# Performance work log

Measured on AMD Instinct MI355X. Metric: run time of the kernel, lower is better.

The kernel has to match this reference:

```python
import jax, jax.numpy as jnp
import numpy as np

B, N, F_IN, HID, OUT = 4096, 116, 116, 256, 2


def setup_inputs() -> dict:
    key = jax.random.key(0)
    ks = jax.random.split(key, 10)
    x = jax.random.normal(ks[0], (B, N, F_IN), dtype=jnp.float32)
    support = jax.random.uniform(ks[1], (B, N, N), dtype=jnp.float32) / N  # row-normalized-ish adjacency
    s = 0.05
    W1 = jax.random.normal(ks[2], (F_IN, HID), dtype=jnp.float32) * s
    b1 = jnp.zeros((HID,), dtype=jnp.float32)
    W2 = jax.random.normal(ks[3], (HID, OUT * 2), dtype=jnp.float32) * s
    b2 = jnp.zeros((OUT * 2,), dtype=jnp.float32)
    Wr1 = jax.random.normal(ks[4], (N * OUT * 2, 64), dtype=jnp.float32) * s
    br1 = jnp.zeros((64,), dtype=jnp.float32)
    Wr2 = jax.random.normal(ks[5], (64, OUT), dtype=jnp.float32) * s
    br2 = jnp.zeros((OUT,), dtype=jnp.float32)
    return {"x": x, "support": support, "W1": W1, "b1": b1, "W2": W2,
            "b2": b2, "Wr1": Wr1, "br1": br1, "Wr2": Wr2, "br2": br2}


def graph_conv(x, support, W, b):
    # GraphConv: activation(support @ (x @ W) + b)
    xw = jnp.einsum('bnf,fh->bnh', x, W)
    h = jnp.einsum('bnm,bmh->bnh', support, xw) + b
    return jax.nn.relu(h)


def reference(x, support, W1, b1, W2, b2, Wr1, br1, Wr2, br2):
    h = graph_conv(x, support, W1, b1)          # [B, N, HID]
    h = graph_conv(h, support, W2, b2)          # [B, N, 2*OUT]
    flat = h.reshape(h.shape[0], -1)            # [B, N*2*OUT]
    r = jax.nn.relu(flat @ Wr1 + br1)           # [B, 64]
    logits = r @ Wr2 + br2                      # [B, OUT]
    return jax.nn.log_softmax(logits, axis=-1)
```

## Files before the change

### kernel.cpp

```cpp
#include <hip/hip_runtime.h>
#include <math.h>


#define BDIM 512

constexpr int Bsz = 4096;
constexpr int Nn  = 116;
constexpr int Fin = 116;
constexpr int HID = 256;
constexpr int SK  = 136;
constexpr int NF4 = 3364;
constexpr int W1T_ELEMS = 256 * SK;
constexpr int W2T_OFF   = W1T_ELEMS;

typedef __bf16 bf16;
typedef __bf16 bf16x4 __attribute__((ext_vector_type(4)));
typedef __bf16 bf16x8 __attribute__((ext_vector_type(8)));
typedef float  floatx4 __attribute__((ext_vector_type(4)));


__global__ __launch_bounds__(1024) void prep_weights(
    const float* __restrict__ W1, const float* __restrict__ W2,
    bf16* __restrict__ WT)
{
  int j = blockIdx.x * 1024 + threadIdx.x;
  if (j < W1T_ELEMS) {
    int h = j / SK, kk = j - h * SK;
    WT[j] = (bf16)((kk < Fin) ? W1[kk * HID + h] : 0.f);
  } else if (j < W1T_ELEMS + 4 * 264) {
    int t = j - W1T_ELEMS;
    int n = t / 264, k = t - n * 264;
    WT[j] = (bf16)((k < HID) ? W2[k * 4 + n] : 0.f);
  }
}

__device__ __forceinline__ void gl2lds16(const void* g, void* l) {
  __builtin_amdgcn_global_load_lds(
      (const __attribute__((address_space(1))) void*)g,
      (__attribute__((address_space(3))) void*)l, 16, 0, 0);
}

__device__ __attribute__((always_inline)) inline void gemm128(
    const bf16* A, const bf16* Bt, floatx4 (&acc)[2][4],
    int wm, int wn, int quad, int l16)
{
#pragma unroll
  for (int ks = 0; ks < 4; ++ks) {
    const int k0 = ks * 32 + quad * 8;
    bf16x8 af[2], bfr[4];
#pragma unroll
    for (int mt = 0; mt < 2; ++mt)
      af[mt] = *(const bf16x8*)&A[(wm + mt * 16 + l16) * SK + k0];
#pragma unroll
    for (int nt = 0; nt < 4; ++nt)
      bfr[nt] = *(const bf16x8*)&Bt[(wn + nt * 16 + l16) * SK + k0];
#pragma unroll
    for (int mt = 0; mt < 2; ++mt)
#pragma unroll
      for (int nt = 0; nt < 4; ++nt)
        acc[mt][nt] = __builtin_amdgcn_mfma_f32_16x16x32_bf16(af[mt], bfr[nt], acc[mt][nt], 0, 0, 0);
  }
}

__device__ __attribute__((always_inline)) inline void gemm128_ra(
    const bf16x8 (&xf)[2][4], const bf16* Bt, floatx4 (&acc)[2][4],
    int wn, int quad, int l16)
{
#pragma unroll
  for (int ks = 0; ks < 4; ++ks) {
    const int k0 = ks * 32 + quad * 8;
    bf16x8 bfr[4];
#pragma unroll
    for (int nt = 0; nt < 4; ++nt)
      bfr[nt] = *(const bf16x8*)&Bt[(wn + nt * 16 + l16) * SK + k0];
#pragma unroll
    for (int mt = 0; mt < 2; ++mt)
#pragma unroll
      for (int nt = 0; nt < 4; ++nt)
        acc[mt][nt] = __builtin_amdgcn_mfma_f32_16x16x32_bf16(xf[mt][ks], bfr[nt], acc[mt][nt], 0, 0, 0);
  }
}

__device__ __attribute__((always_inline)) inline void zero_acc(floatx4 (&acc)[2][4])
{
#pragma unroll
  for (int mt = 0; mt < 2; ++mt)
#pragma unroll
    for (int nt = 0; nt < 4; ++nt) { acc[mt][nt][0]=acc[mt][nt][1]=acc[mt][nt][2]=acc[mt][nt][3]=0.f; }
}

__global__ __launch_bounds__(BDIM, 4) void gcn_fused(
    const float* __restrict__ X, const float* __restrict__ SUPP,
    const bf16* __restrict__ WT,
    const float* __restrict__ B1v, const float* __restrict__ B2v,
    const float* __restrict__ Wr1, const float* __restrict__ br1,
    const float* __restrict__ Wr2, const float* __restrict__ br2,
    float* __restrict__ OUTP)
{
  __shared__ __align__(16) bf16 ssup[128 * SK];
  __shared__ __align__(16) bf16 swb [128 * SK];
  __shared__ __align__(16) bf16 sw2t[4 * 264];
  __shared__ __align__(16) bf16 stt [4 * SK];
  __shared__ float sh2[464];
  __shared__ float spart[8 * 64];

  const int b    = blockIdx.x;
  const int tid  = threadIdx.x;
  const int wid  = tid >> 6;
  const int lane = tid & 63;
  const int quad = lane >> 4;
  const int l16  = lane & 15;

  const int wm = (wid & 3) * 32;
  const int wn = (wid >> 2) * 64;

  {
    const char* wg = (const char*)WT;
    char* wl = (char*)swb;
    for (int off = wid * 1024; off < 34816; off += 8 * 1024)
      gl2lds16(wg + off + lane * 16, wl + off);
    if (wid == 7) {
      const char* w2g = (const char*)(WT + W2T_OFF);
      char* w2l = (char*)sw2t;
      gl2lds16(w2g + lane * 16, w2l);
      gl2lds16(w2g + 1024 + lane * 16, w2l + 1024);
      if (lane < 4) gl2lds16(w2g + 2048 + lane * 16, w2l + 2048);
    }
  }

  const float* xrow = X + (size_t)b * (Nn * Fin);
  bf16x8 xf[2][4];
#pragma unroll
  for (int mt = 0; mt < 2; ++mt) {
    const int row = wm + mt * 16 + l16;
    const bool rv = row < Nn;
    const float* pr = xrow + (rv ? row : 0) * Fin;
#pragma unroll
    for (int ks = 0; ks < 4; ++ks) {
      const int k0 = ks * 32 + quad * 8;
      float4 u0 = make_float4(0.f, 0.f, 0.f, 0.f);
      float4 u1 = make_float4(0.f, 0.f, 0.f, 0.f);
      if (ks < 3 || quad < 3) u0 = *(const float4*)(pr + k0);
      if (ks < 3 || quad < 2) u1 = *(const float4*)(pr + k0 + 4);
      bf16x8 f;
      f[0]=(bf16)u0.x; f[1]=(bf16)u0.y; f[2]=(bf16)u0.z; f[3]=(bf16)u0.w;
      f[4]=(bf16)u1.x; f[5]=(bf16)u1.y; f[6]=(bf16)u1.z; f[7]=(bf16)u1.w;
      bf16x8 z; 
#pragma unroll
      for (int j = 0; j < 8; ++j) z[j] = (bf16)0.f;
      xf[mt][ks] = rv ? f : z;
    }
  }

  {
    const float4* sg = (const float4*)(SUPP + (size_t)b * (Nn * Nn));
    for (int i = tid; i < NF4; i += BDIM) {
      int m  = i / 29;
      int kq = (i - m * 29) * 4;
      float4 u = sg[i];
      bf16x4 q; q[0]=(bf16)u.x; q[1]=(bf16)u.y; q[2]=(bf16)u.z; q[3]=(bf16)u.w;
      *(bf16x4*)&ssup[m * SK + kq] = q;
    }
    bf16x4 z; z[0]=z[1]=z[2]=z[3]=(bf16)0.f;
    for (int i = tid; i < 128 * 5; i += BDIM) {
      int m = i / 5, cc = 116 + (i - m * 5) * 4;
      *(bf16x4*)&ssup[m * SK + cc] = z;
    }
    for (int i = tid; i < 12 * 29; i += BDIM) {
      int r = 116 + i / 29, cc = (i - (i / 29) * 29) * 4;
      *(bf16x4*)&ssup[r * SK + cc] = z;
    }
  }
  asm volatile("s_waitcnt vmcnt(0)" ::: "memory");
  __syncthreads();

  floatx4 acc[2][4];
  bf16x4  xwb0[2][4], xwb1[2][4];

  zero_acc(acc);
  gemm128_ra(xf, swb, acc, wn, quad, l16);
#pragma unroll
  for (int mt = 0; mt < 2; ++mt)
#pragma unroll
    for (int nt = 0; nt < 4; ++nt) {
      floatx4 a = acc[mt][nt];
      bf16x4 p; p[0]=(bf16)a[0]; p[1]=(bf16)a[1]; p[2]=(bf16)a[2]; p[3]=(bf16)a[3];
      xwb0[mt][nt] = p;
    }
  __syncthreads();

  {
    const char* wg = (const char*)(WT + 128 * SK);
    char* wl = (char*)swb;
    for (int off = wid * 1024; off < 34816; off += 8 * 1024)
      gl2lds16(wg + off + lane * 16, wl + off);
  }
  asm volatile("s_waitcnt vmcnt(0)" ::: "memory");
  __syncthreads();

  zero_acc(acc);
  gemm128_ra(xf, swb, acc, wn, quad, l16);
#pragma unroll
  for (int mt = 0; mt < 2; ++mt)
#pragma unroll
    for (int nt = 0; nt < 4; ++nt) {
      floatx4 a = acc[mt][nt];
      bf16x4 p; p[0]=(bf16)a[0]; p[1]=(bf16)a[1]; p[2]=(bf16)a[2]; p[3]=(bf16)a[3];
      xwb1[mt][nt] = p;
    }
  __syncthreads();

#pragma unroll
  for (int mt = 0; mt < 2; ++mt)
#pragma unroll
    for (int nt = 0; nt < 4; ++nt) {
      int mb = wm + mt * 16 + quad * 4;
      int n  = wn + nt * 16 + l16;
      *(bf16x4*)&swb[n * SK + mb] = xwb0[mt][nt];
    }
  __syncthreads();

  floatx4 acc3; acc3[0]=acc3[1]=acc3[2]=acc3[3]=0.f;

#pragma unroll
  for (int c = 0; c < 2; ++c) {
    zero_acc(acc);
    gemm128(ssup, swb, acc, wm, wn, quad, l16);
    __syncthreads();

#pragma unroll
    for (int mt = 0; mt < 2; ++mt)
#pragma unroll
      for (int nt = 0; nt < 4; ++nt) {
        int mb   = wm + mt * 16 + quad * 4;
        int coll = wn + nt * 16 + l16;
        float bb = B1v[c * 128 + coll];
        floatx4 a = acc[mt][nt];
#pragma unroll
        for (int r = 0; r < 4; ++r)
          swb[(mb + r) * SK + coll] = (bf16)fmaxf(a[r] + bb, 0.f);
      }
    __syncthreads();

#pragma unroll
    for (int ks = 0; ks < 4; ++ks) {
      const int k0 = ks * 32 + quad * 8;
      bf16x8 bfr = *(const bf16x8*)&sw2t[(l16 & 3) * 264 + c * 128 + k0];
      bf16x8 af  = *(const bf16x8*)&swb[(wid * 16 + l16) * SK + k0];
      acc3 = __builtin_amdgcn_mfma_f32_16x16x32_bf16(af, bfr, acc3, 0, 0, 0);
    }
    if (c == 0) {
      __syncthreads();
#pragma unroll
      for (int mt = 0; mt < 2; ++mt)
#pragma unroll
        for (int nt = 0; nt < 4; ++nt) {
          int mb = wm + mt * 16 + quad * 4;
          int n  = wn + nt * 16 + l16;
          *(bf16x4*)&swb[n * SK + mb] = xwb1[mt][nt];
        }
      __syncthreads();
    }
  }

  {
    int mb = wid * 16 + quad * 4;
    bf16x4 p;
    if (mb < Nn) { p[0]=(bf16)acc3[0]; p[1]=(bf16)acc3[1]; p[2]=(bf16)acc3[2]; p[3]=(bf16)acc3[3]; }
    else         { p[0]=p[1]=p[2]=p[3]=(bf16)0.f; }
    if (l16 < 4) *(bf16x4*)&stt[l16 * SK + mb] = p;
  }
  __syncthreads();

  floatx4 acc4; acc4[0]=acc4[1]=acc4[2]=acc4[3]=0.f;
#pragma unroll
  for (int ks = 0; ks < 4; ++ks) {
    const int k0 = ks * 32 + quad * 8;
    bf16x8 af  = *(const bf16x8*)&ssup[(wid * 16 + l16) * SK + k0];
    bf16x8 bfr = *(const bf16x8*)&stt[(l16 & 3) * SK + k0];
    acc4 = __builtin_amdgcn_mfma_f32_16x16x32_bf16(af, bfr, acc4, 0, 0, 0);
  }
  if (l16 < 4) {
    float bb = B2v[l16];
#pragma unroll
    for (int r = 0; r < 4; ++r) {
      int m = wid * 16 + quad * 4 + r;
      if (m < Nn) sh2[m * 4 + l16] = fmaxf(acc4[r] + bb, 0.f);
    }
  }
  __syncthreads();

  {
    int j   = tid & 63;
    int ksl = tid >> 6;
    int kb  = ksl * 58;
    float p = 0.f;
#pragma unroll 4
    for (int kk = 0; kk < 58; ++kk)
      p = fmaf(sh2[kb + kk], Wr1[(kb + kk) * 64 + j], p);
    spart[ksl * 64 + j] = p;
  }
  __syncthreads();
  if (tid < 64) {
    int j = tid;
    float r = 0.f;
#pragma unroll
    for (int s = 0; s < 8; ++s) r += spart[s * 64 + j];
    r = fmaxf(r + br1[j], 0.f);
    float p0 = r * Wr2[j * 2 + 0];
    float p1 = r * Wr2[j * 2 + 1];
#pragma unroll
    for (int off = 32; off > 0; off >>= 1) {
      p0 += __shfl_xor(p0, off, 64);
      p1 += __shfl_xor(p1, off, 64);
    }
    float l0 = p0 + br2[0], l1 = p1 + br2[1];
    float mx  = fmaxf(l0, l1);
    float lse = mx + logf(expf(l0 - mx) + expf(l1 - mx));
    if (j < 2) OUTP[(size_t)b * 2 + j] = (j ? l1 : l0) - lse;
  }
}

extern "C" void kernel_launch(void* const* d_in, const int* in_sizes, int n_in,
                              void* d_out, int out_size, void* d_ws, size_t ws_size,
                              hipStream_t stream) {
  const float* X    = (const float*)d_in[0];
  const float* SUPP = (const float*)d_in[1];
  const float* W1   = (const float*)d_in[2];
  const float* B1v  = (const float*)d_in[3];
  const float* W2   = (const float*)d_in[4];
  const float* B2v  = (const float*)d_in[5];
  const float* Wr1  = (const float*)d_in[6];
  const float* br1  = (const float*)d_in[7];
  const float* Wr2  = (const float*)d_in[8];
  const float* br2  = (const float*)d_in[9];
  bf16* WT = (bf16*)d_ws;

  prep_weights<<<36, 1024, 0, stream>>>(W1, W2, WT);
  gcn_fused<<<Bsz, BDIM, 0, stream>>>(X, SUPP, WT, B1v, B2v,
                                      Wr1, br1, Wr2, br2, (float*)d_out);
}
```

Baseline: 551.8 us.

## Read weight B-fragments directly from global memory instead of staging in LDS

The first GEMM's transposed W1 fragments and the W2 fragments are now loaded straight from global memory (L2-resident) into registers, with all 16 fragments per half prefetched before the MFMAs. The LDS staging via global_load_lds, its waitcnt and several barriers are removed, and the sw2t buffer is dropped. The support-matrix load is moved to the start and unrolled with clamped indices. This removes LDS traffic and synchronisation between the weight copy and the GEMM, at the cost of more global/L2 loads per wave and higher register pressure from the bfr[4][4] prefetch.

Measured after the change: 555.0 us. No clear change (+0.6%).

```diff
diff --git a/kernel.cpp b/kernel.cpp
--- a/kernel.cpp
+++ b/kernel.cpp
@@ -34,12 +34,6 @@
   }
 }
 
-__device__ __forceinline__ void gl2lds16(const void* g, void* l) {
-  __builtin_amdgcn_global_load_lds(
-      (const __attribute__((address_space(1))) void*)g,
-      (__attribute__((address_space(3))) void*)l, 16, 0, 0);
-}
-
 __device__ __attribute__((always_inline)) inline void gemm128(
     const bf16* A, const bf16* Bt, floatx4 (&acc)[2][4],
     int wm, int wn, int quad, int l16)
@@ -62,23 +56,25 @@
   }
 }
 
-__device__ __attribute__((always_inline)) inline void gemm128_ra(
-    const bf16x8 (&xf)[2][4], const bf16* Bt, floatx4 (&acc)[2][4],
+__device__ __attribute__((always_inline)) inline void gemm128_gb(
+    const bf16x8 (&xf)[2][4], const bf16* __restrict__ Bg, floatx4 (&acc)[2][4],
     int wn, int quad, int l16)
 {
+  bf16x8 bfr[4][4];
 #pragma unroll
   for (int ks = 0; ks < 4; ++ks) {
     const int k0 = ks * 32 + quad * 8;
-    bf16x8 bfr[4];
 #pragma unroll
     for (int nt = 0; nt < 4; ++nt)
-      bfr[nt] = *(const bf16x8*)&Bt[(wn + nt * 16 + l16) * SK + k0];
+      bfr[ks][nt] = *(const bf16x8*)&Bg[(wn + nt * 16 + l16) * SK + k0];
+  }
+#pragma unroll
+  for (int ks = 0; ks < 4; ++ks)
 #pragma unroll
     for (int mt = 0; mt < 2; ++mt)
 #pragma unroll
       for (int nt = 0; nt < 4; ++nt)
-        acc[mt][nt] = __builtin_amdgcn_mfma_f32_16x16x32_bf16(xf[mt][ks], bfr[nt], acc[mt][nt], 0, 0, 0);
-  }
+        acc[mt][nt] = __builtin_amdgcn_mfma_f32_16x16x32_bf16(xf[mt][ks], bfr[ks][nt], acc[mt][nt], 0, 0, 0);
 }
 
 __device__ __attribute__((always_inline)) inline void zero_acc(floatx4 (&acc)[2][4])
@@ -99,7 +95,6 @@
 {
   __shared__ __align__(16) bf16 ssup[128 * SK];
   __shared__ __align__(16) bf16 swb [128 * SK];
-  __shared__ __align__(16) bf16 sw2t[4 * 264];
   __shared__ __align__(16) bf16 stt [4 * SK];
   __shared__ float sh2[464];
   __shared__ float spart[8 * 64];
@@ -115,16 +110,25 @@
   const int wn = (wid >> 2) * 64;
 
   {
-    const char* wg = (const char*)WT;
-    char* wl = (char*)swb;
-    for (int off = wid * 1024; off < 34816; off += 8 * 1024)
-      gl2lds16(wg + off + lane * 16, wl + off);
-    if (wid == 7) {
-      const char* w2g = (const char*)(WT + W2T_OFF);
-      char* w2l = (char*)sw2t;
-      gl2lds16(w2g + lane * 16, w2l);
-      gl2lds16(w2g + 1024 + lane * 16, w2l + 1024);
-      if (lane < 4) gl2lds16(w2g + 2048 + lane * 16, w2l + 2048);
+    const float4* sg = (const float4*)(SUPP + (size_t)b * (Nn * Nn));
+#pragma unroll
+    for (int it = 0; it < 7; ++it) {
+      int i  = tid + it * BDIM;
+      int ic = (i < NF4) ? i : (NF4 - 1);
+      int m  = ic / 29;
+      int kq = (ic - m * 29) * 4;
+      float4 u = sg[ic];
+      bf16x4 q; q[0]=(bf16)u.x; q[1]=(bf16)u.y; q[2]=(bf16)u.z; q[3]=(bf16)u.w;
+      *(bf16x4*)&ssup[m * SK + kq] = q;
+    }
+    bf16x4 z; z[0]=z[1]=z[2]=z[3]=(bf16)0.f;
+    for (int i = tid; i < 128 * 5; i += BDIM) {
+      int m = i / 5, cc = 116 + (i - m * 5) * 4;
+      *(bf16x4*)&ssup[m * SK + cc] = z;
+    }
+    for (int i = tid; i < 12 * 29; i += BDIM) {
+      int r = 116 + i / 29, cc = (i - (i / 29) * 29) * 4;
+      *(bf16x4*)&ssup[r * SK + cc] = z;
     }
   }
 
@@ -145,61 +149,31 @@
       bf16x8 f;
       f[0]=(bf16)u0.x; f[1]=(bf16)u0.y; f[2]=(bf16)u0.z; f[3]=(bf16)u0.w;
       f[4]=(bf16)u1.x; f[5]=(bf16)u1.y; f[6]=(bf16)u1.z; f[7]=(bf16)u1.w;
-      bf16x8 z; 
-#pragma unroll
-      for (int j = 0; j < 8; ++j) z[j] = (bf16)0.f;
-      xf[mt][ks] = rv ? f : z;
-    }
-  }
-
-  {
-    const float4* sg = (const float4*)(SUPP + (size_t)b * (Nn * Nn));
-    for (int i = tid; i < NF4; i += BDIM) {
-      int m  = i / 29;
-      int kq = (i - m * 29) * 4;
-      float4 u = sg[i];
-      bf16x4 q; q[0]=(bf16)u.x; q[1]=(bf16)u.y; q[2]=(bf16)u.z; q[3]=(bf16)u.w;
-      *(bf16x4*)&ssup[m * SK + kq] = q;
-    }
-    bf16x4 z; z[0]=z[1]=z[2]=z[3]=(bf16)0.f;
-    for (int i = tid; i < 128 * 5; i += BDIM) {
-      int m = i / 5, cc = 116 + (i - m * 5) * 4;
-      *(bf16x4*)&ssup[m * SK + cc] = z;
-    }
-    for (int i = tid; i < 12 * 29; i += BDIM) {
-      int r = 116 + i / 29, cc = (i - (i / 29) * 29) * 4;
-      *(bf16x4*)&ssup[r * SK + cc] = z;
-    }
-  }
-  asm volatile("s_waitcnt vmcnt(0)" ::: "memory");
-  __syncthreads();
+      bf16x8 zz;
+#pragma unroll
+      for (int j = 0; j < 8; ++j) zz[j] = (bf16)0.f;
+      xf[mt][ks] = rv ? f : zz;
+    }
+  }
 
   floatx4 acc[2][4];
-  bf16x4  xwb0[2][4], xwb1[2][4];
+  bf16x4  xwb1[2][4];
 
   zero_acc(acc);
-  gemm128_ra(xf, swb, acc, wn, quad, l16);
+  gemm128_gb(xf, WT, acc, wn, quad, l16);
 #pragma unroll
   for (int mt = 0; mt < 2; ++mt)
 #pragma unroll
     for (int nt = 0; nt < 4; ++nt) {
+      int mb = wm + mt * 16 + quad * 4;
+      int n  = wn + nt * 16 + l16;
       floatx4 a = acc[mt][nt];
       bf16x4 p; p[0]=(bf16)a[0]; p[1]=(bf16)a[1]; p[2]=(bf16)a[2]; p[3]=(bf16)a[3];
-      xwb0[mt][nt] = p;
-    }
-  __syncthreads();
-
-  {
-    const char* wg = (const char*)(WT + 128 * SK);
-    char* wl = (char*)swb;
-    for (int off = wid * 1024; off < 34816; off += 8 * 1024)
-      gl2lds16(wg + off + lane * 16, wl + off);
-  }
-  asm volatile("s_waitcnt vmcnt(0)" ::: "memory");
-  __syncthreads();
+      *(bf16x4*)&swb[n * SK + mb] = p;
+    }
 
   zero_acc(acc);
-  gemm128_ra(xf, swb, acc, wn, quad, l16);
+  gemm128_gb(xf, WT + 128 * SK, acc, wn, quad, l16);
 #pragma unroll
   for (int mt = 0; mt < 2; ++mt)
 #pragma unroll
@@ -207,16 +181,6 @@
       floatx4 a = acc[mt][nt];
       bf16x4 p; p[0]=(bf16)a[0]; p[1]=(bf16)a[1]; p[2]=(bf16)a[2]; p[3]=(bf16)a[3];
       xwb1[mt][nt] = p;
-    }
-  __syncthreads();
-
-#pragma unroll
-  for (int mt = 0; mt < 2; ++mt)
-#pragma unroll
-    for (int nt = 0; nt < 4; ++nt) {
-      int mb = wm + mt * 16 + quad * 4;
-      int n  = wn + nt * 16 + l16;
-      *(bf16x4*)&swb[n * SK + mb] = xwb0[mt][nt];
     }
   __syncthreads();
 
@@ -245,7 +209,7 @@
 #pragma unroll
     for (int ks = 0; ks < 4; ++ks) {
       const int k0 = ks * 32 + quad * 8;
-      bf16x8 bfr = *(const bf16x8*)&sw2t[(l16 & 3) * 264 + c * 128 + k0];
+      bf16x8 bfr = *(const bf16x8*)&WT[W2T_OFF + (l16 & 3) * 264 + c * 128 + k0];
       bf16x8 af  = *(const bf16x8*)&swb[(wid * 16 + l16) * SK + k0];
       acc3 = __builtin_amdgcn_mfma_f32_16x16x32_bf16(af, bfr, acc3, 0, 0, 0);
     }
```
